# Performance work log

Measured on AMD Instinct MI355X. Metric: run time of the kernel, lower is better.

The kernel has to match this reference:

```python
import jax, jax.numpy as jnp
import numpy as np

B, H, S, D = 2, 8, 2048, 64
N_HASHES = 6
EPS = 1e-8


def setup_inputs() -> dict:
    key = jax.random.key(0)
    kq, kk, kv, kr = jax.random.split(key, 4)
    Q = jax.random.normal(kq, (B, H, S, D), dtype=jnp.float32)
    K = jax.random.normal(kk, (B, H, S, D), dtype=jnp.float32)
    V = jax.random.normal(kv, (B, H, S, D), dtype=jnp.float32)
    rotations = jax.random.normal(kr, (H, N_HASHES, D), dtype=jnp.float32)
    return {"Q": Q, "K": K, "V": V, "rotations": rotations}


def _buckets(X, rotations, powers):
    # X: [b,h,l,d] -> integer bucket id per position, [b,h,l]
    Xn = X / (jnp.linalg.norm(X, axis=-1, keepdims=True) + 1e-8)
    bits = jnp.einsum('bhld,hnd->bhln', Xn, rotations) > 0
    return jnp.sum(bits.astype(jnp.int32) * powers, axis=-1)


def reference(Q, K, V, rotations):
    n_hashes = rotations.shape[1]
    d = Q.shape[-1]
    powers = (2 ** jnp.arange(n_hashes)).astype(jnp.int32)
    q_buckets = _buckets(Q, rotations, powers)  # [b,h,sq]
    k_buckets = _buckets(K, rotations, powers)  # [b,h,sk]
    # queries only attend to keys whose full hash code matches exactly
    match = q_buckets[..., :, None] == k_buckets[..., None, :]  # [b,h,sq,sk]
    scores = jnp.einsum('bhqd,bhkd->bhqk', Q, K) / (d ** 0.5)
    row_has = jnp.any(match, axis=-1, keepdims=True)
    masked = jnp.where(match, scores, -jnp.inf)
    m = jnp.max(masked, axis=-1, keepdims=True)
    m = jnp.where(row_has, m, 0.0)  # avoid -inf for empty rows
    e = jnp.where(match, jnp.exp(scores - m), 0.0)
    weights = e / (jnp.sum(e, axis=-1, keepdims=True) + EPS)
    out = jnp.einsum('bhqk,bhkd->bhqd', weights, V)
    return out / n_hashes
```

## Files before the change

### kernel.cpp

```cpp
#include <hip/hip_runtime.h>
#include <math.h>


constexpr int S_LEN = 2048;
constexpr int D = 64;
constexpr int NHASH = 6;
constexpr int BH = 16;
constexpr int NB = 64;
constexpr int QPAD = 4;
constexpr int PADQ = S_LEN + (QPAD - 1) * NB;
constexpr int NGRP = PADQ / QPAD;
constexpr int NBLK = NGRP / 4;
constexpr int GSTRIDE = 37;
constexpr size_t KTP_OFF = 1u << 20;
constexpr size_t VTP_OFF = KTP_OFF + ((size_t)BH * 16 * S_LEN * 4 * 4);

__global__ __launch_bounds__(1024) void lsh_buckets2(const float* __restrict__ Q,
                                                     const float* __restrict__ K,
                                                     const float* __restrict__ rot,
                                                     int* __restrict__ qb,
                                                     int* __restrict__ kb) {
    const int gw   = blockIdx.x * 16 + (threadIdx.x >> 6);
    const int lane = threadIdx.x & 63;
    const bool isK = gw >= BH * S_LEN;
    const int wid  = isK ? gw - BH * S_LEN : gw;
    const float* X = isK ? K : Q;
    int* dst       = isK ? kb : qb;
    const int h    = (wid >> 11) & 7;

    const float x  = X[(size_t)wid * D + lane];
    const float* r = rot + (size_t)h * NHASH * D + lane;
    float p0 = x * r[0 * D], p1 = x * r[1 * D], p2 = x * r[2 * D];
    float p3 = x * r[3 * D], p4 = x * r[4 * D], p5 = x * r[5 * D];
#pragma unroll
    for (int off = 32; off >= 1; off >>= 1) {
        p0 += __shfl_xor(p0, off, 64);
        p1 += __shfl_xor(p1, off, 64);
        p2 += __shfl_xor(p2, off, 64);
        p3 += __shfl_xor(p3, off, 64);
        p4 += __shfl_xor(p4, off, 64);
        p5 += __shfl_xor(p5, off, 64);
    }
    int bucket = (p0 > 0.f ? 1 : 0) | (p1 > 0.f ? 2 : 0) | (p2 > 0.f ? 4 : 0) |
                 (p3 > 0.f ? 8 : 0) | (p4 > 0.f ? 16 : 0) | (p5 > 0.f ? 32 : 0);
    if (lane == 0) dst[wid] = bucket;
}

__global__ __launch_bounds__(256) void lsh_sortfuse32(const int* __restrict__ qbuckets,
                                                      const int* __restrict__ kbuckets,
                                                      int* __restrict__ q_plist,
                                                      int* __restrict__ k_list) {
    __shared__ int hist[NB];
    __shared__ int cur[NB];
    __shared__ int kst[NB], kcnt[NB];
    __shared__ int qst[NB];
    __shared__ int total;
    const int which = blockIdx.x >> 4;
    const int bh    = blockIdx.x & 15;
    const int tid   = threadIdx.x;

    if (which) {
        if (tid < NB) hist[tid] = 0;
        __syncthreads();
        int myk[8];
#pragma unroll
        for (int i = 0; i < 8; ++i) {
            myk[i] = kbuckets[bh * S_LEN + i * 256 + tid];
            atomicAdd(&hist[myk[i]], 1);
        }
        __syncthreads();
        if (tid < NB) {
            const int cnt = hist[tid];
            int x = cnt;
#pragma unroll
            for (int off = 1; off < 64; off <<= 1) {
                const int y = __shfl_up(x, off, 64);
                if (tid >= off) x += y;
            }
            cur[tid] = x - cnt;
        }
        __syncthreads();
        int* klp = k_list + bh * S_LEN;
#pragma unroll
        for (int i = 0; i < 8; ++i) {
            const int b    = myk[i];
            const int slot = atomicAdd(&cur[b], 1);
            klp[slot] = i * 256 + tid;
        }
    } else {
        if (tid < NB) hist[tid] = 0;
        __syncthreads();
#pragma unroll
        for (int i = 0; i < 8; ++i)
            atomicAdd(&hist[kbuckets[bh * S_LEN + i * 256 + tid]], 1);
        __syncthreads();
        if (tid < NB) {
            const int cnt = hist[tid];
            int x = cnt;
#pragma unroll
            for (int off = 1; off < 64; off <<= 1) {
                const int y = __shfl_up(x, off, 64);
                if (tid >= off) x += y;
            }
            kst[tid]  = x - cnt;
            kcnt[tid] = cnt;
        }
        __syncthreads();

        if (tid < NB) hist[tid] = 0;
        __syncthreads();
        int myq[8];
#pragma unroll
        for (int i = 0; i < 8; ++i) {
            myq[i] = qbuckets[bh * S_LEN + i * 256 + tid];
            atomicAdd(&hist[myq[i]], 1);
        }
        __syncthreads();
        if (tid < NB) {
            const int cnt = hist[tid];
            const int v   = (cnt + QPAD - 1) & ~(QPAD - 1);
            int x = v;
#pragma unroll
            for (int off = 1; off < 64; off <<= 1) {
                const int y = __shfl_up(x, off, 64);
                if (tid >= off) x += y;
            }
            qst[tid] = x - v;
            cur[tid] = x - v;
            if (tid == 63) total = x;
        }
        __syncthreads();

        int* qp = q_plist + bh * PADQ;
        if (tid < NB) {
            const int cnt    = hist[tid];
            const int padded = (cnt + QPAD - 1) & ~(QPAD - 1);
            const int sent   = 0xFFFF | (kcnt[tid] << 16);
            for (int t = qst[tid] + cnt; t < qst[tid] + padded; ++t) qp[t] = sent;
        }
        for (int t = total + tid; t < PADQ; t += 256) qp[t] = -1;
#pragma unroll
        for (int i = 0; i < 8; ++i) {
            const int b    = myq[i];
            const int slot = atomicAdd(&cur[b], 1);
            const int pos  = slot & 3;
            int e = i * 256 + tid;
            if (pos == 0)      e |= kst[b] << 16;
            else if (pos == 1) e |= kcnt[b] << 16;
            qp[slot] = e;
        }
    }
}

__global__ __launch_bounds__(256) void lsh_packkv(const float* __restrict__ K,
                                                  const float* __restrict__ V,
                                                  const int* __restrict__ k_list,
                                                  float* __restrict__ Ktp,
                                                  float* __restrict__ Vtp) {
    const int gw   = (blockIdx.x * 256 + threadIdx.x) >> 6;
    const int lane = threadIdx.x & 63;
    const int bh   = gw >> 9;
    const int s0   = (gw & 511) * 4;
    const float* Kb = K + (size_t)bh * S_LEN * D;
    const float* Vb = V + (size_t)bh * S_LEN * D;
    const int* kl   = k_list + bh * S_LEN;
    float* kt       = Ktp + (size_t)bh * 16 * S_LEN * 4;
    float* vt       = Vtp + (size_t)bh * S_LEN * D;
    const int dblk  = lane >> 2, dj = lane & 3;
#pragma unroll
    for (int j = 0; j < 4; ++j) {
        const int slot = s0 + j;
        const int kidx = kl[slot];
        kt[((size_t)dblk * S_LEN + slot) * 4 + dj] = Kb[(size_t)kidx * D + lane];
        vt[(size_t)slot * D + lane]                = Vb[(size_t)kidx * D + lane];
    }
}

__global__ __launch_bounds__(256) void lsh_attn_pv(const float* __restrict__ Q,
                                                   const float* __restrict__ Ktp,
                                                   const float* __restrict__ Vtp,
                                                   const int* __restrict__ q_plist,
                                                   float* __restrict__ out) {
    __shared__ float wbuf[4][QPAD][64];

    const int wv   = threadIdx.x >> 6;
    const int lane = threadIdx.x & 63;
    const int w    = blockIdx.x;
    const int bh   = (w & 7) + 8 * ((w >> 3) & 1);
    const int gb   = ((w >> 4) * GSTRIDE) % NBLK;
    const int grp  = gb * 4 + wv;

    const int* pl = q_plist + bh * PADQ + 4 * grp;
    const int e0 = __builtin_amdgcn_readfirstlane(pl[0]);
    if ((e0 & 0xFFFF) == 0xFFFF) return;
    const int e1 = __builtin_amdgcn_readfirstlane(pl[1]);
    const int e2 = __builtin_amdgcn_readfirstlane(pl[2]);
    const int e3 = __builtin_amdgcn_readfirstlane(pl[3]);

    const int q0 = e0 & 0xFFFF;
    const int ks = (unsigned)e0 >> 16;
    const int nk = (unsigned)e1 >> 16;
    const int t1 = e1 & 0xFFFF, t2 = e2 & 0xFFFF, t3 = e3 & 0xFFFF;
    const bool v1 = t1 != 0xFFFF, v2 = t2 != 0xFFFF, v3 = t3 != 0xFFFF;
    const int q1 = v1 ? t1 : q0;
    const int q2 = v2 ? t2 : q0;
    const int q3 = v3 ? t3 : q0;

    float* outb = out + (size_t)bh * S_LEN * D;
    if (nk == 0) {
        outb[(size_t)q0 * D + lane] = 0.0f;
        if (v1) outb[(size_t)q1 * D + lane] = 0.0f;
        if (v2) outb[(size_t)q2 * D + lane] = 0.0f;
        if (v3) outb[(size_t)q3 * D + lane] = 0.0f;
        return;
    }

    const float* ktb  = Ktp + (size_t)bh * 16 * S_LEN * 4;
    const float* vtb  = Vtp + (size_t)bh * S_LEN * D;
    const float* qr0  = Q + ((size_t)bh * S_LEN + q0) * D;
    const float* qr1  = Q + ((size_t)bh * S_LEN + q1) * D;
    const float* qr2  = Q + ((size_t)bh * S_LEN + q2) * D;
    const float* qr3  = Q + ((size_t)bh * S_LEN + q3) * D;

    float l0 = 0.f, l1 = 0.f, l2 = 0.f, l3 = 0.f;
    float acc0 = 0.f, acc1 = 0.f, acc2 = 0.f, acc3 = 0.f;

    for (int c = 0; c * 64 < nk; ++c) {
        const int cnk  = min(64, nk - c * 64);
        const int cl   = min(lane, cnk - 1);
        const int slot = ks + c * 64 + cl;

        float s0 = 0.f, s1 = 0.f, s2 = 0.f, s3 = 0.f;
#pragma unroll
        for (int d4 = 0; d4 < 16; ++d4) {
            const float4 kv = *(const float4*)(ktb + ((size_t)d4 * S_LEN + slot) * 4);
            const float4 a  = *(const float4*)(qr0 + d4 * 4);
            const float4 b  = *(const float4*)(qr1 + d4 * 4);
            const float4 cq = *(const float4*)(qr2 + d4 * 4);
            const float4 dq = *(const float4*)(qr3 + d4 * 4);
            s0 += a.x * kv.x + a.y * kv.y + a.z * kv.z + a.w * kv.w;
            s1 += b.x * kv.x + b.y * kv.y + b.z * kv.z + b.w * kv.w;
            s2 += cq.x * kv.x + cq.y * kv.y + cq.z * kv.z + cq.w * kv.w;
            s3 += dq.x * kv.x + dq.y * kv.y + dq.z * kv.z + dq.w * kv.w;
        }

        const bool kvalid = lane < cnk;
        const float ea = kvalid ? __expf(s0 * 0.125f) : 0.f;
        const float eb = kvalid ? __expf(s1 * 0.125f) : 0.f;
        const float ec = kvalid ? __expf(s2 * 0.125f) : 0.f;
        const float ed = kvalid ? __expf(s3 * 0.125f) : 0.f;
        l0 += ea; l1 += eb; l2 += ec; l3 += ed;
        wbuf[wv][0][lane] = ea;
        wbuf[wv][1][lane] = eb;
        wbuf[wv][2][lane] = ec;
        wbuf[wv][3][lane] = ed;

        const float* vrow = vtb + (size_t)(ks + c * 64) * D;
        const int ng = (cnk + 3) >> 2;
        for (int g = 0; g < ng; ++g) {
            const float4 eA = *(const float4*)&wbuf[wv][0][g * 4];
            const float4 eB = *(const float4*)&wbuf[wv][1][g * 4];
            const float4 eC = *(const float4*)&wbuf[wv][2][g * 4];
            const float4 eD = *(const float4*)&wbuf[wv][3][g * 4];
            const float vx = vrow[(g * 4 + 0) * D + lane];
            const float vy = vrow[(g * 4 + 1) * D + lane];
            const float vz = vrow[(g * 4 + 2) * D + lane];
            const float vw = vrow[(g * 4 + 3) * D + lane];
            acc0 += eA.x * vx + eA.y * vy + eA.z * vz + eA.w * vw;
            acc1 += eB.x * vx + eB.y * vy + eB.z * vz + eB.w * vw;
            acc2 += eC.x * vx + eC.y * vy + eC.z * vz + eC.w * vw;
            acc3 += eD.x * vx + eD.y * vy + eD.z * vz + eD.w * vw;
        }
    }

#pragma unroll
    for (int off = 32; off >= 1; off >>= 1) {
        l0 += __shfl_xor(l0, off, 64);
        l1 += __shfl_xor(l1, off, 64);
        l2 += __shfl_xor(l2, off, 64);
        l3 += __shfl_xor(l3, off, 64);
    }

    const float inv6 = 1.0f / 6.0f;
    outb[(size_t)q0 * D + lane] = acc0 / (l0 + 1e-8f) * inv6;
    if (v1) outb[(size_t)q1 * D + lane] = acc1 / (l1 + 1e-8f) * inv6;
    if (v2) outb[(size_t)q2 * D + lane] = acc2 / (l2 + 1e-8f) * inv6;
    if (v3) outb[(size_t)q3 * D + lane] = acc3 / (l3 + 1e-8f) * inv6;
}

__global__ __launch_bounds__(256) void lsh_attn_g(const float* __restrict__ Q,
                                                  const float* __restrict__ K,
                                                  const float* __restrict__ V,
                                                  const int* __restrict__ q_plist,
                                                  const int* __restrict__ k_list,
                                                  float* __restrict__ out) {
    __shared__ float wbuf[4][QPAD][64];
    __shared__ int   kbuf[4][64];

    const int wv   = threadIdx.x >> 6;
    const int lane = threadIdx.x & 63;
    const int w    = blockIdx.x;
    const int bh   = (w & 7) + 8 * ((w >> 3) & 1);
    const int gb   = ((w >> 4) * GSTRIDE) % NBLK;
    const int grp  = gb * 4 + wv;

    const int* pl = q_plist + bh * PADQ + 4 * grp;
    const int e0 = __builtin_amdgcn_readfirstlane(pl[0]);
    if ((e0 & 0xFFFF) == 0xFFFF) return;
    const int e1 = __builtin_amdgcn_readfirstlane(pl[1]);
    const int e2 = __builtin_amdgcn_readfirstlane(pl[2]);
    const int e3 = __builtin_amdgcn_readfirstlane(pl[3]);

    const int q0 = e0 & 0xFFFF;
    const int ks = (unsigned)e0 >> 16;
    const int nk = (unsigned)e1 >> 16;
    const int t1 = e1 & 0xFFFF, t2 = e2 & 0xFFFF, t3 = e3 & 0xFFFF;
    const bool v1 = t1 != 0xFFFF, v2 = t2 != 0xFFFF, v3 = t3 != 0xFFFF;
    const int q1 = v1 ? t1 : q0;
    const int q2 = v2 ? t2 : q0;
    const int q3 = v3 ? t3 : q0;

    float* outb = out + (size_t)bh * S_LEN * D;
    if (nk == 0) {
        outb[(size_t)q0 * D + lane] = 0.0f;
        if (v1) outb[(size_t)q1 * D + lane] = 0.0f;
        if (v2) outb[(size_t)q2 * D + lane] = 0.0f;
        if (v3) outb[(size_t)q3 * D + lane] = 0.0f;
        return;
    }

    const int* kl     = k_list + bh * S_LEN + ks;
    const float* Kb   = K + (size_t)bh * S_LEN * D;
    const float* Vb   = V + (size_t)bh * S_LEN * D;
    const float* qr0  = Q + ((size_t)bh * S_LEN + q0) * D;
    const float* qr1  = Q + ((size_t)bh * S_LEN + q1) * D;
    const float* qr2  = Q + ((size_t)bh * S_LEN + q2) * D;
    const float* qr3  = Q + ((size_t)bh * S_LEN + q3) * D;

    float l0 = 0.f, l1 = 0.f, l2 = 0.f, l3 = 0.f;
    float acc0 = 0.f, acc1 = 0.f, acc2 = 0.f, acc3 = 0.f;

    for (int c = 0; c * 64 < nk; ++c) {
        const int cnk  = min(64, nk - c * 64);
        const int kidx = kl[c * 64 + min(lane, cnk - 1)];
        const float* krow = Kb + (size_t)kidx * D;

        float s0 = 0.f, s1 = 0.f, s2 = 0.f, s3 = 0.f;
#pragma unroll
        for (int d4 = 0; d4 < 16; ++d4) {
            const float4 kv = *(const float4*)(krow + d4 * 4);
            const float4 a  = *(const float4*)(qr0 + d4 * 4);
            const float4 b  = *(const float4*)(qr1 + d4 * 4);
            const float4 cq = *(const float4*)(qr2 + d4 * 4);
            const float4 dq = *(const float4*)(qr3 + d4 * 4);
            s0 += a.x * kv.x + a.y * kv.y + a.z * kv.z + a.w * kv.w;
            s1 += b.x * kv.x + b.y * kv.y + b.z * kv.z + b.w * kv.w;
            s2 += cq.x * kv.x + cq.y * kv.y + cq.z * kv.z + cq.w * kv.w;
            s3 += dq.x * kv.x + dq.y * kv.y + dq.z * kv.z + dq.w * kv.w;
        }

        const bool kvalid = lane < cnk;
        const float ea = kvalid ? __expf(s0 * 0.125f) : 0.f;
        const float eb = kvalid ? __expf(s1 * 0.125f) : 0.f;
        const float ec = kvalid ? __expf(s2 * 0.125f) : 0.f;
        const float ed = kvalid ? __expf(s3 * 0.125f) : 0.f;
        l0 += ea; l1 += eb; l2 += ec; l3 += ed;
        wbuf[wv][0][lane] = ea;
        wbuf[wv][1][lane] = eb;
        wbuf[wv][2][lane] = ec;
        wbuf[wv][3][lane] = ed;
        kbuf[wv][lane]    = kidx;

        const int ng = (cnk + 3) >> 2;
        for (int g = 0; g < ng; ++g) {
            const int4   kk = *(const int4*)&kbuf[wv][g * 4];
            const float4 eA = *(const float4*)&wbuf[wv][0][g * 4];
            const float4 eB = *(const float4*)&wbuf[wv][1][g * 4];
            const float4 eC = *(const float4*)&wbuf[wv][2][g * 4];
            const float4 eD = *(const float4*)&wbuf[wv][3][g * 4];
            const float vx = Vb[(size_t)kk.x * D + lane];
            const float vy = Vb[(size_t)kk.y * D + lane];
            const float vz = Vb[(size_t)kk.z * D + lane];
            const float vw = Vb[(size_t)kk.w * D + lane];
            acc0 += eA.x * vx + eA.y * vy + eA.z * vz + eA.w * vw;
            acc1 += eB.x * vx + eB.y * vy + eB.z * vz + eB.w * vw;
            acc2 += eC.x * vx + eC.y * vy + eC.z * vz + eC.w * vw;
            acc3 += eD.x * vx + eD.y * vy + eD.z * vz + eD.w * vw;
        }
    }

#pragma unroll
    for (int off = 32; off >= 1; off >>= 1) {
        l0 += __shfl_xor(l0, off, 64);
        l1 += __shfl_xor(l1, off, 64);
        l2 += __shfl_xor(l2, off, 64);
        l3 += __shfl_xor(l3, off, 64);
    }

    const float inv6 = 1.0f / 6.0f;
    outb[(size_t)q0 * D + lane] = acc0 / (l0 + 1e-8f) * inv6;
    if (v1) outb[(size_t)q1 * D + lane] = acc1 / (l1 + 1e-8f) * inv6;
    if (v2) outb[(size_t)q2 * D + lane] = acc2 / (l2 + 1e-8f) * inv6;
    if (v3) outb[(size_t)q3 * D + lane] = acc3 / (l3 + 1e-8f) * inv6;
}

extern "C" void kernel_launch(void* const* d_in, const int* in_sizes, int n_in,
                              void* d_out, int out_size, void* d_ws, size_t ws_size,
                              hipStream_t stream) {
    const float* Q   = (const float*)d_in[0];
    const float* K   = (const float*)d_in[1];
    const float* V   = (const float*)d_in[2];
    const float* rot = (const float*)d_in[3];
    float* out = (float*)d_out;

    char* ws = (char*)d_ws;
    int* q_buckets = (int*)(ws);
    int* k_buckets = (int*)(ws + 131072);
    int* k_list    = (int*)(ws + 262144);
    int* q_plist   = (int*)(ws + 393216);

    const size_t pack_bytes = (size_t)BH * S_LEN * D * sizeof(float);
    const bool packed = ws_size >= VTP_OFF + pack_bytes + 16384;
    float* Ktp = (float*)(ws + KTP_OFF);
    float* Vtp = (float*)(ws + VTP_OFF);

    lsh_buckets2<<<2 * BH * S_LEN / 16, 1024, 0, stream>>>(Q, K, rot, q_buckets, k_buckets);
    lsh_sortfuse32<<<32, 256, 0, stream>>>(q_buckets, k_buckets, q_plist, k_list);
    if (packed) {
        lsh_packkv<<<BH * S_LEN / 16, 256, 0, stream>>>(K, V, k_list, Ktp, Vtp);
        lsh_attn_pv<<<NBLK * BH, 256, 0, stream>>>(Q, Ktp, Vtp, q_plist, out);
    } else {
        lsh_attn_g<<<NBLK * BH, 256, 0, stream>>>(Q, K, V, q_plist, k_list, out);
    }
}
```

Measured before the change: 74.85 us.

## Group eight queries per wave with Q staged in LDS

```diff
diff --git a/kernel.cpp b/kernel.cpp
--- a/kernel.cpp
+++ b/kernel.cpp
@@ -7,20 +7,20 @@
 constexpr int NHASH = 6;
 constexpr int BH = 16;
 constexpr int NB = 64;
-constexpr int QPAD = 4;
+constexpr int QPAD = 8;
 constexpr int PADQ = S_LEN + (QPAD - 1) * NB;
 constexpr int NGRP = PADQ / QPAD;
 constexpr int NBLK = NGRP / 4;
-constexpr int GSTRIDE = 37;
+constexpr int GSTRIDE = 35;
 constexpr size_t KTP_OFF = 1u << 20;
 constexpr size_t VTP_OFF = KTP_OFF + ((size_t)BH * 16 * S_LEN * 4 * 4);
 
-__global__ __launch_bounds__(1024) void lsh_buckets2(const float* __restrict__ Q,
-                                                     const float* __restrict__ K,
-                                                     const float* __restrict__ rot,
-                                                     int* __restrict__ qb,
-                                                     int* __restrict__ kb) {
-    const int gw   = blockIdx.x * 16 + (threadIdx.x >> 6);
+__global__ __launch_bounds__(256) void lsh_buckets2(const float* __restrict__ Q,
+                                                    const float* __restrict__ K,
+                                                    const float* __restrict__ rot,
+                                                    int* __restrict__ qb,
+                                                    int* __restrict__ kb) {
+    const int gw   = (blockIdx.x * 256 + threadIdx.x) >> 6;
     const int lane = threadIdx.x & 63;
     const bool isK = gw >= BH * S_LEN;
     const int wid  = isK ? gw - BH * S_LEN : gw;
@@ -143,7 +143,7 @@
         for (int i = 0; i < 8; ++i) {
             const int b    = myq[i];
             const int slot = atomicAdd(&cur[b], 1);
-            const int pos  = slot & 3;
+            const int pos  = slot & (QPAD - 1);
             int e = i * 256 + tid;
             if (pos == 0)      e |= kst[b] << 16;
             else if (pos == 1) e |= kcnt[b] << 16;
@@ -176,11 +176,12 @@
     }
 }
 
-__global__ __launch_bounds__(256) void lsh_attn_pv(const float* __restrict__ Q,
-                                                   const float* __restrict__ Ktp,
-                                                   const float* __restrict__ Vtp,
-                                                   const int* __restrict__ q_plist,
-                                                   float* __restrict__ out) {
+__global__ __launch_bounds__(256) void lsh_attn_pv8(const float* __restrict__ Q,
+                                                    const float* __restrict__ Ktp,
+                                                    const float* __restrict__ Vtp,
+                                                    const int* __restrict__ q_plist,
+                                                    float* __restrict__ out) {
+    __shared__ float qlds[4][QPAD][64];
     __shared__ float wbuf[4][QPAD][64];
 
     const int wv   = threadIdx.x >> 6;
@@ -190,110 +191,110 @@
     const int gb   = ((w >> 4) * GSTRIDE) % NBLK;
     const int grp  = gb * 4 + wv;
 
-    const int* pl = q_plist + bh * PADQ + 4 * grp;
+    const int* pl = q_plist + bh * PADQ + QPAD * grp;
     const int e0 = __builtin_amdgcn_readfirstlane(pl[0]);
     if ((e0 & 0xFFFF) == 0xFFFF) return;
     const int e1 = __builtin_amdgcn_readfirstlane(pl[1]);
-    const int e2 = __builtin_amdgcn_readfirstlane(pl[2]);
-    const int e3 = __builtin_amdgcn_readfirstlane(pl[3]);
-
-    const int q0 = e0 & 0xFFFF;
     const int ks = (unsigned)e0 >> 16;
     const int nk = (unsigned)e1 >> 16;
-    const int t1 = e1 & 0xFFFF, t2 = e2 & 0xFFFF, t3 = e3 & 0xFFFF;
-    const bool v1 = t1 != 0xFFFF, v2 = t2 != 0xFFFF, v3 = t3 != 0xFFFF;
-    const int q1 = v1 ? t1 : q0;
-    const int q2 = v2 ? t2 : q0;
-    const int q3 = v3 ? t3 : q0;
+
+    int qi[QPAD];
+    bool vq[QPAD];
+    qi[0] = e0 & 0xFFFF;
+    vq[0] = true;
+    {
+        const int t1 = e1 & 0xFFFF;
+        vq[1] = t1 != 0xFFFF;
+        qi[1] = vq[1] ? t1 : qi[0];
+    }
+#pragma unroll
+    for (int j = 2; j < QPAD; ++j) {
+        const int ej = __builtin_amdgcn_readfirstlane(pl[j]);
+        const int tj = ej & 0xFFFF;
+        vq[j] = tj != 0xFFFF;
+        qi[j] = vq[j] ? tj : qi[0];
+    }
 
     float* outb = out + (size_t)bh * S_LEN * D;
     if (nk == 0) {
-        outb[(size_t)q0 * D + lane] = 0.0f;
-        if (v1) outb[(size_t)q1 * D + lane] = 0.0f;
-        if (v2) outb[(size_t)q2 * D + lane] = 0.0f;
-        if (v3) outb[(size_t)q3 * D + lane] = 0.0f;
+#pragma unroll
+        for (int j = 0; j < QPAD; ++j)
+            if (vq[j]) outb[(size_t)qi[j] * D + lane] = 0.0f;
         return;
     }
 
-    const float* ktb  = Ktp + (size_t)bh * 16 * S_LEN * 4;
-    const float* vtb  = Vtp + (size_t)bh * S_LEN * D;
-    const float* qr0  = Q + ((size_t)bh * S_LEN + q0) * D;
-    const float* qr1  = Q + ((size_t)bh * S_LEN + q1) * D;
-    const float* qr2  = Q + ((size_t)bh * S_LEN + q2) * D;
-    const float* qr3  = Q + ((size_t)bh * S_LEN + q3) * D;
-
-    float l0 = 0.f, l1 = 0.f, l2 = 0.f, l3 = 0.f;
-    float acc0 = 0.f, acc1 = 0.f, acc2 = 0.f, acc3 = 0.f;
+    const float* ktb = Ktp + (size_t)bh * 16 * S_LEN * 4;
+    const float* vtb = Vtp + (size_t)bh * S_LEN * D;
+    const float* Qb  = Q + (size_t)bh * S_LEN * D;
+
+#pragma unroll
+    for (int j = 0; j < QPAD; ++j)
+        qlds[wv][j][lane] = Qb[(size_t)qi[j] * D + lane];
+
+    float l[QPAD], acc[QPAD];
+#pragma unroll
+    for (int j = 0; j < QPAD; ++j) { l[j] = 0.f; acc[j] = 0.f; }
 
     for (int c = 0; c * 64 < nk; ++c) {
         const int cnk  = min(64, nk - c * 64);
         const int cl   = min(lane, cnk - 1);
         const int slot = ks + c * 64 + cl;
 
-        float s0 = 0.f, s1 = 0.f, s2 = 0.f, s3 = 0.f;
+        float s[QPAD];
+#pragma unroll
+        for (int j = 0; j < QPAD; ++j) s[j] = 0.f;
 #pragma unroll
         for (int d4 = 0; d4 < 16; ++d4) {
             const float4 kv = *(const float4*)(ktb + ((size_t)d4 * S_LEN + slot) * 4);
-            const float4 a  = *(const float4*)(qr0 + d4 * 4);
-            const float4 b  = *(const float4*)(qr1 + d4 * 4);
-            const float4 cq = *(const float4*)(qr2 + d4 * 4);
-            const float4 dq = *(const float4*)(qr3 + d4 * 4);
-            s0 += a.x * kv.x + a.y * kv.y + a.z * kv.z + a.w * kv.w;
-            s1 += b.x * kv.x + b.y * kv.y + b.z * kv.z + b.w * kv.w;
-            s2 += cq.x * kv.x + cq.y * kv.y + cq.z * kv.z + cq.w * kv.w;
-            s3 += dq.x * kv.x + dq.y * kv.y + dq.z * kv.z + dq.w * kv.w;
+#pragma unroll
+            for (int j = 0; j < QPAD; ++j) {
+                const float4 qv = *(const float4*)&qlds[wv][j][d4 * 4];
+                s[j] += qv.x * kv.x + qv.y * kv.y + qv.z * kv.z + qv.w * kv.w;
+            }
         }
 
         const bool kvalid = lane < cnk;
-        const float ea = kvalid ? __expf(s0 * 0.125f) : 0.f;
-        const float eb = kvalid ? __expf(s1 * 0.125f) : 0.f;
-        const float ec = kvalid ? __expf(s2 * 0.125f) : 0.f;
-        const float ed = kvalid ? __expf(s3 * 0.125f) : 0.f;
-        l0 += ea; l1 += eb; l2 += ec; l3 += ed;
-        wbuf[wv][0][lane] = ea;
-        wbuf[wv][1][lane] = eb;
-        wbuf[wv][2][lane] = ec;
-        wbuf[wv][3][lane] = ed;
+#pragma unroll
+        for (int j = 0; j < QPAD; ++j) {
+            const float e = kvalid ? __expf(s[j] * 0.125f) : 0.f;
+            l[j] += e;
+            wbuf[wv][j][lane] = e;
+        }
 
         const float* vrow = vtb + (size_t)(ks + c * 64) * D;
         const int ng = (cnk + 3) >> 2;
         for (int g = 0; g < ng; ++g) {
-            const float4 eA = *(const float4*)&wbuf[wv][0][g * 4];
-            const float4 eB = *(const float4*)&wbuf[wv][1][g * 4];
-            const float4 eC = *(const float4*)&wbuf[wv][2][g * 4];
-            const float4 eD = *(const float4*)&wbuf[wv][3][g * 4];
             const float vx = vrow[(g * 4 + 0) * D + lane];
             const float vy = vrow[(g * 4 + 1) * D + lane];
             const float vz = vrow[(g * 4 + 2) * D + lane];
             const float vw = vrow[(g * 4 + 3) * D + lane];
-            acc0 += eA.x * vx + eA.y * vy + eA.z * vz + eA.w * vw;
-            acc1 += eB.x * vx + eB.y * vy + eB.z * vz + eB.w * vw;
-            acc2 += eC.x * vx + eC.y * vy + eC.z * vz + eC.w * vw;
-            acc3 += eD.x * vx + eD.y * vy + eD.z * vz + eD.w * vw;
+#pragma unroll
+            for (int j = 0; j < QPAD; ++j) {
+                const float4 e4 = *(const float4*)&wbuf[wv][j][g * 4];
+                acc[j] += e4.x * vx + e4.y * vy + e4.z * vz + e4.w * vw;
+            }
         }
     }
 
 #pragma unroll
     for (int off = 32; off >= 1; off >>= 1) {
-        l0 += __shfl_xor(l0, off, 64);
-        l1 += __shfl_xor(l1, off, 64);
-        l2 += __shfl_xor(l2, off, 64);
-        l3 += __shfl_xor(l3, off, 64);
+#pragma unroll
+        for (int j = 0; j < QPAD; ++j) l[j] += __shfl_xor(l[j], off, 64);
     }
 
     const float inv6 = 1.0f / 6.0f;
-    outb[(size_t)q0 * D + lane] = acc0 / (l0 + 1e-8f) * inv6;
-    if (v1) outb[(size_t)q1 * D + lane] = acc1 / (l1 + 1e-8f) * inv6;
-    if (v2) outb[(size_t)q2 * D + lane] = acc2 / (l2 + 1e-8f) * inv6;
-    if (v3) outb[(size_t)q3 * D + lane] = acc3 / (l3 + 1e-8f) * inv6;
-}
-
-__global__ __launch_bounds__(256) void lsh_attn_g(const float* __restrict__ Q,
-                                                  const float* __restrict__ K,
-                                                  const float* __restrict__ V,
-                                                  const int* __restrict__ q_plist,
-                                                  const int* __restrict__ k_list,
-                                                  float* __restrict__ out) {
+#pragma unroll
+    for (int j = 0; j < QPAD; ++j)
+        if (vq[j]) outb[(size_t)qi[j] * D + lane] = acc[j] / (l[j] + 1e-8f) * inv6;
+}
+
+__global__ __launch_bounds__(256) void lsh_attn_g8(const float* __restrict__ Q,
+                                                   const float* __restrict__ K,
+                                                   const float* __restrict__ V,
+                                                   const int* __restrict__ q_plist,
+                                                   const int* __restrict__ k_list,
+                                                   float* __restrict__ out) {
+    __shared__ float qlds[4][QPAD][64];
     __shared__ float wbuf[4][QPAD][64];
     __shared__ int   kbuf[4][64];
 
@@ -304,104 +305,103 @@
     const int gb   = ((w >> 4) * GSTRIDE) % NBLK;
     const int grp  = gb * 4 + wv;
 
-    const int* pl = q_plist + bh * PADQ + 4 * grp;
+    const int* pl = q_plist + bh * PADQ + QPAD * grp;
     const int e0 = __builtin_amdgcn_readfirstlane(pl[0]);
     if ((e0 & 0xFFFF) == 0xFFFF) return;
     const int e1 = __builtin_amdgcn_readfirstlane(pl[1]);
-    const int e2 = __builtin_amdgcn_readfirstlane(pl[2]);
-    const int e3 = __builtin_amdgcn_readfirstlane(pl[3]);
-
-    const int q0 = e0 & 0xFFFF;
     const int ks = (unsigned)e0 >> 16;
     const int nk = (unsigned)e1 >> 16;
-    const int t1 = e1 & 0xFFFF, t2 = e2 & 0xFFFF, t3 = e3 & 0xFFFF;
-    const bool v1 = t1 != 0xFFFF, v2 = t2 != 0xFFFF, v3 = t3 != 0xFFFF;
-    const int q1 = v1 ? t1 : q0;
-    const int q2 = v2 ? t2 : q0;
-    const int q3 = v3 ? t3 : q0;
+
+    int qi[QPAD];
+    bool vq[QPAD];
+    qi[0] = e0 & 0xFFFF;
+    vq[0] = true;
+    {
+        const int t1 = e1 & 0xFFFF;
+        vq[1] = t1 != 0xFFFF;
+        qi[1] = vq[1] ? t1 : qi[0];
+    }
+#pragma unroll
+    for (int j = 2; j < QPAD; ++j) {
+        const int ej = __builtin_amdgcn_readfirstlane(pl[j]);
+        const int tj = ej & 0xFFFF;
+        vq[j] = tj != 0xFFFF;
+        qi[j] = vq[j] ? tj : qi[0];
+    }
 
     float* outb = out + (size_t)bh * S_LEN * D;
     if (nk == 0) {
-        outb[(size_t)q0 * D + lane] = 0.0f;
-        if (v1) outb[(size_t)q1 * D + lane] = 0.0f;
-        if (v2) outb[(size_t)q2 * D + lane] = 0.0f;
-        if (v3) outb[(size_t)q3 * D + lane] = 0.0f;
+#pragma unroll
+        for (int j = 0; j < QPAD; ++j)
+            if (vq[j]) outb[(size_t)qi[j] * D + lane] = 0.0f;
         return;
     }
 
-    const int* kl     = k_list + bh * S_LEN + ks;
-    const float* Kb   = K + (size_t)bh * S_LEN * D;
-    const float* Vb   = V + (size_t)bh * S_LEN * D;
-    const float* qr0  = Q + ((size_t)bh * S_LEN + q0) * D;
-    const float* qr1  = Q + ((size_t)bh * S_LEN + q1) * D;
-    const float* qr2  = Q + ((size_t)bh * S_LEN + q2) * D;
-    const float* qr3  = Q + ((size_t)bh * S_LEN + q3) * D;
-
-    float l0 = 0.f, l1 = 0.f, l2 = 0.f, l3 = 0.f;
-    float acc0 = 0.f, acc1 = 0.f, acc2 = 0.f, acc3 = 0.f;
+    const int* kl   = k_list + bh * S_LEN + ks;
+    const float* Kb = K + (size_t)bh * S_LEN * D;
+    const float* Vb = V + (size_t)bh * S_LEN * D;
+    const float* Qb = Q + (size_t)bh * S_LEN * D;
+
+#pragma unroll
+    for (int j = 0; j < QPAD; ++j)
+        qlds[wv][j][lane] = Qb[(size_t)qi[j] * D + lane];
+
+    float l[QPAD], acc[QPAD];
+#pragma unroll
+    for (int j = 0; j < QPAD; ++j) { l[j] = 0.f; acc[j] = 0.f; }
 
     for (int c = 0; c * 64 < nk; ++c) {
         const int cnk  = min(64, nk - c * 64);
         const int kidx = kl[c * 64 + min(lane, cnk - 1)];
         const float* krow = Kb + (size_t)kidx * D;
 
-        float s0 = 0.f, s1 = 0.f, s2 = 0.f, s3 = 0.f;
+        float s[QPAD];
+#pragma unroll
+        for (int j = 0; j < QPAD; ++j) s[j] = 0.f;
 #pragma unroll
         for (int d4 = 0; d4 < 16; ++d4) {
             const float4 kv = *(const float4*)(krow + d4 * 4);
-            const float4 a  = *(const float4*)(qr0 + d4 * 4);
-            const float4 b  = *(const float4*)(qr1 + d4 * 4);
-            const float4 cq = *(const float4*)(qr2 + d4 * 4);
-            const float4 dq = *(const float4*)(qr3 + d4 * 4);
-            s0 += a.x * kv.x + a.y * kv.y + a.z * kv.z + a.w * kv.w;
-            s1 += b.x * kv.x + b.y * kv.y + b.z * kv.z + b.w * kv.w;
-            s2 += cq.x * kv.x + cq.y * kv.y + cq.z * kv.z + cq.w * kv.w;
-            s3 += dq.x * kv.x + dq.y * kv.y + dq.z * kv.z + dq.w * kv.w;
+#pragma unroll
+            for (int j = 0; j < QPAD; ++j) {
+                const float4 qv = *(const float4*)&qlds[wv][j][d4 * 4];
+                s[j] += qv.x * kv.x + qv.y * kv.y + qv.z * kv.z + qv.w * kv.w;
+            }
         }
 
         const bool kvalid = lane < cnk;
-        const float ea = kvalid ? __expf(s0 * 0.125f) : 0.f;
-        const float eb = kvalid ? __expf(s1 * 0.125f) : 0.f;
-        const float ec = kvalid ? __expf(s2 * 0.125f) : 0.f;
-        const float ed = kvalid ? __expf(s3 * 0.125f) : 0.f;
-        l0 += ea; l1 += eb; l2 += ec; l3 += ed;
-        wbuf[wv][0][lane] = ea;
-        wbuf[wv][1][lane] = eb;
-        wbuf[wv][2][lane] = ec;
-        wbuf[wv][3][lane] = ed;
-        kbuf[wv][lane]    = kidx;
+#pragma unroll
+        for (int j = 0; j < QPAD; ++j) {
+            const float e = kvalid ? __expf(s[j] * 0.125f) : 0.f;
+            l[j] += e;
+            wbuf[wv][j][lane] = e;
+        }
+        kbuf[wv][lane] = kidx;
 
         const int ng = (cnk + 3) >> 2;
         for (int g = 0; g < ng; ++g) {
-            const int4   kk = *(const int4*)&kbuf[wv][g * 4];
-            const float4 eA = *(const float4*)&wbuf[wv][0][g * 4];
-            const float4 eB = *(const float4*)&wbuf[wv][1][g * 4];
-            const float4 eC = *(const float4*)&wbuf[wv][2][g * 4];
-            const float4 eD = *(const float4*)&wbuf[wv][3][g * 4];
+            const int4 kk = *(const int4*)&kbuf[wv][g * 4];
             const float vx = Vb[(size_t)kk.x * D + lane];
             const float vy = Vb[(size_t)kk.y * D + lane];
             const float vz = Vb[(size_t)kk.z * D + lane];
             const float vw = Vb[(size_t)kk.w * D + lane];
-            acc0 += eA.x * vx + eA.y * vy + eA.z * vz + eA.w * vw;
-            acc1 += eB.x * vx + eB.y * vy + eB.z * vz + eB.w * vw;
-            acc2 += eC.x * vx + eC.y * vy + eC.z * vz + eC.w * vw;
-            acc3 += eD.x * vx + eD.y * vy + eD.z * vz + eD.w * vw;
+#pragma unroll
+            for (int j = 0; j < QPAD; ++j) {
+                const float4 e4 = *(const float4*)&wbuf[wv][j][g * 4];
+                acc[j] += e4.x * vx + e4.y * vy + e4.z * vz + e4.w * vw;
+            }
         }
     }
 
 #pragma unroll
     for (int off = 32; off >= 1; off >>= 1) {
-        l0 += __shfl_xor(l0, off, 64);
-        l1 += __shfl_xor(l1, off, 64);
-        l2 += __shfl_xor(l2, off, 64);
-        l3 += __shfl_xor(l3, off, 64);
+#pragma unroll
+        for (int j = 0; j < QPAD; ++j) l[j] += __shfl_xor(l[j], off, 64);
     }
 
     const float inv6 = 1.0f / 6.0f;
-    outb[(size_t)q0 * D + lane] = acc0 / (l0 + 1e-8f) * inv6;
-    if (v1) outb[(size_t)q1 * D + lane] = acc1 / (l1 + 1e-8f) * inv6;
-    if (v2) outb[(size_t)q2 * D + lane] = acc2 / (l2 + 1e-8f) * inv6;
-    if (v3) outb[(size_t)q3 * D + lane] = acc3 / (l3 + 1e-8f) * inv6;
+#pragma unroll
+    for (int j = 0; j < QPAD; ++j)
+        if (vq[j]) outb[(size_t)qi[j] * D + lane] = acc[j] / (l[j] + 1e-8f) * inv6;
 }
 
 extern "C" void kernel_launch(void* const* d_in, const int* in_sizes, int n_in,
@@ -424,12 +424,12 @@
     float* Ktp = (float*)(ws + KTP_OFF);
     float* Vtp = (float*)(ws + VTP_OFF);
 
-    lsh_buckets2<<<2 * BH * S_LEN / 16, 1024, 0, stream>>>(Q, K, rot, q_buckets, k_buckets);
+    lsh_buckets2<<<2 * BH * S_LEN / 4, 256, 0, stream>>>(Q, K, rot, q_buckets, k_buckets);
     lsh_sortfuse32<<<32, 256, 0, stream>>>(q_buckets, k_buckets, q_plist, k_list);
     if (packed) {
         lsh_packkv<<<BH * S_LEN / 16, 256, 0, stream>>>(K, V, k_list, Ktp, Vtp);
-        lsh_attn_pv<<<NBLK * BH, 256, 0, stream>>>(Q, Ktp, Vtp, q_plist, out);
+        lsh_attn_pv8<<<NBLK * BH, 256, 0, stream>>>(Q, Ktp, Vtp, q_plist, out);
     } else {
-        lsh_attn_g<<<NBLK * BH, 256, 0, stream>>>(Q, K, V, q_plist, k_list, out);
-    }
-}
+        lsh_attn_g8<<<NBLK * BH, 256, 0, stream>>>(Q, K, V, q_plist, k_list, out);
+    }
+}
```

Result: slower. 109.7 us (+46.6%).
